# Optimization experiments

Hardware: AMD Instinct MI355X
Metric: run time of the kernel (lower is better)

Reference implementation:

```python
import jax, jax.numpy as jnp
import numpy as np

# ---- module hyperparams (match init_kwargs) ----
REGIONS_DIMS = [0, 1, 2, 4, 9, 16]
ALL_DIM = sum(REGIONS_DIMS)          # 32
NUM_REGIONS = len(REGIONS_DIMS)      # 6
FIELD_NUM = 32
VOCAB = 200000
BATCH = 8192
TEMPERATURE = 1.0
EPS = 1e-5                            # torch BatchNorm1d default eps


def _build_region_mask():
    """Replicates init_variables(): row 0 is all-zero (drop-feature region),
    rows 1..R-1 are disjoint consecutive segments of sizes REGIONS_DIMS[1:]."""
    mask = np.zeros((NUM_REGIONS, ALL_DIM), dtype=np.float32)
    dims_pre_sum = [0] + [sum(REGIONS_DIMS[1:i]) for i in range(2, NUM_REGIONS)]
    for r, (pre, dim) in enumerate(zip(dims_pre_sum, REGIONS_DIMS[1:]), start=1):
        mask[r, pre:pre + dim] = 1.0
    return jnp.asarray(mask)


def setup_inputs() -> dict:
    key = jax.random.key(0)
    k_ids, k_emb, k_w = jax.random.split(key, 3)
    input_ids = jax.random.randint(k_ids, (BATCH, FIELD_NUM), 0, VOCAB, dtype=jnp.int64)
    # torch.nn.init.uniform_(a=-0.05, b=0.05)
    emb_table = jax.random.uniform(k_emb, (VOCAB, ALL_DIM), dtype=jnp.float32,
                                   minval=-0.05, maxval=0.05)
    # xavier_uniform on [F, R, 1]: bound = sqrt(6/(R+1))
    bound = float(np.sqrt(6.0 / (NUM_REGIONS + 1)))
    field_region_weights = jax.random.uniform(
        k_w, (FIELD_NUM, NUM_REGIONS, 1), dtype=jnp.float32, minval=-bound, maxval=bound)
    return {
        "input_ids": input_ids,
        "emb_table": emb_table,
        "field_region_weights": field_region_weights,
        "region_mask": _build_region_mask(),
    }


def reference(input_ids, emb_table, field_region_weights, region_mask):
    # Embedding gather: [B, F, D]
    emb = emb_table[input_ids]
    # BatchNorm1d(field_num, affine=False), training mode: per-field stats over (batch, D),
    # biased variance (torch normalizes with biased var).
    mean = jnp.mean(emb, axis=(0, 2), keepdims=True)
    var = jnp.var(emb, axis=(0, 2), keepdims=True)
    x = (emb - mean) * jax.lax.rsqrt(var + EPS)
    # softmax over regions: [F, R]
    w = jax.nn.softmax(field_region_weights[..., 0] / TEMPERATURE, axis=1)
    # sum_r w[f,r] * mask[r,d] -> per-(field, dim) scale; equivalent to the original's
    # broadcast-to-[B,F,R,D], multiply, and sum over R, without the big intermediate.
    coef = jnp.einsum('fr,rd->fd', w, region_mask)
    return x * coef[None, :, :]
```

## Files before the change

kernel.cpp:

```cpp
#include <hip/hip_runtime.h>
#include <math.h>

#define BATCH    8192
#define FIELDS   32
#define DIM      32
#define NREG     6
#define EPS      1e-5f


__global__ void irazor_init_kernel(const float* __restrict__ frw,
                                   const float* __restrict__ mask,
                                   float* __restrict__ ws) {
    const int t = threadIdx.x;
    if (t < 64) ws[t] = 0.0f;
    __shared__ float smask[NREG * DIM];
    if (t < NREG * DIM) smask[t] = mask[t];
    __syncthreads();
    if (t < FIELDS) {
        float w[NREG];
        float m = -1e30f;
        #pragma unroll
        for (int r = 0; r < NREG; ++r) {
            w[r] = frw[t * NREG + r];
            m = fmaxf(m, w[r]);
        }
        float s = 0.0f;
        #pragma unroll
        for (int r = 0; r < NREG; ++r) { w[r] = __expf(w[r] - m); s += w[r]; }
        const float inv = 1.0f / s;
        for (int d = 0; d < DIM; ++d) {
            float c = 0.0f;
            #pragma unroll
            for (int r = 0; r < NREG; ++r) c += w[r] * smask[r * DIM + d];
            ws[64 + t * DIM + d] = c * inv;
        }
    }
}

__global__ __launch_bounds__(256) void irazor_stats_kernel(
        const int* __restrict__ ids,
        const float* __restrict__ table,
        float* __restrict__ ws) {
    const int f    = blockIdx.y;
    const int b0   = blockIdx.x * 256;
    const int t    = threadIdx.x;
    const int rsub = t >> 3;
    const int vec  = t & 7;

    float s = 0.0f, sq = 0.0f;
    #pragma unroll
    for (int i = 0; i < 8; ++i) {
        const int b  = b0 + i * 32 + rsub;
        const int id = ids[b * FIELDS + f];
        const float4 v = *reinterpret_cast<const float4*>(
            table + (size_t)id * DIM + vec * 4);
        s  += v.x + v.y + v.z + v.w;
        sq += v.x * v.x + v.y * v.y + v.z * v.z + v.w * v.w;
    }

    #pragma unroll
    for (int off = 1; off < 64; off <<= 1) {
        s  += __shfl_xor(s, off);
        sq += __shfl_xor(sq, off);
    }
    __shared__ float ls[4], lq[4];
    const int wave = t >> 6;
    if ((t & 63) == 0) { ls[wave] = s; lq[wave] = sq; }
    __syncthreads();
    if (t == 0) {
        const float S  = ls[0] + ls[1] + ls[2] + ls[3];
        const float SQ = lq[0] + lq[1] + lq[2] + lq[3];
        atomicAdd(&ws[f], S);
        atomicAdd(&ws[32 + f], SQ);
    }
}

__global__ __launch_bounds__(256) void irazor_out_kernel(
        const int* __restrict__ ids,
        const float* __restrict__ table,
        const float* __restrict__ ws,
        float* __restrict__ out) {
    const float* __restrict__ coef = ws + 64;
    const float invN = 1.0f / (float)(BATCH * DIM);
    const size_t total = (size_t)BATCH * FIELDS * (DIM / 4);
    for (size_t e = (size_t)blockIdx.x * blockDim.x + threadIdx.x; e < total;
         e += (size_t)gridDim.x * blockDim.x) {
        const int r   = (int)(e >> 3);
        const int vec = (int)(e & 7);
        const int f   = r & (FIELDS - 1);
        const int id  = ids[r];
        const float4 v = *reinterpret_cast<const float4*>(
            table + (size_t)id * DIM + vec * 4);
        const float S    = ws[f];
        const float SQ   = ws[32 + f];
        const float mean = S * invN;
        const float var  = SQ * invN - mean * mean;
        const float istd = rsqrtf(var + EPS);
        const float4 c = *reinterpret_cast<const float4*>(coef + f * DIM + vec * 4);
        float4 o;
        o.x = (v.x - mean) * istd * c.x;
        o.y = (v.y - mean) * istd * c.y;
        o.z = (v.z - mean) * istd * c.z;
        o.w = (v.w - mean) * istd * c.w;
        reinterpret_cast<float4*>(out)[e] = o;
    }
}

extern "C" void kernel_launch(void* const* d_in, const int* in_sizes, int n_in,
                              void* d_out, int out_size, void* d_ws, size_t ws_size,
                              hipStream_t stream) {
    const int*   ids   = (const int*)d_in[0];
    const float* table = (const float*)d_in[1];
    const float* frw   = (const float*)d_in[2];
    const float* mask  = (const float*)d_in[3];
    float*       out   = (float*)d_out;
    float*       ws    = (float*)d_ws;

    irazor_init_kernel<<<1, 256, 0, stream>>>(frw, mask, ws);

    dim3 sgrid(BATCH / 256, FIELDS);
    irazor_stats_kernel<<<sgrid, 256, 0, stream>>>(ids, table, ws);

    irazor_out_kernel<<<2048, 256, 0, stream>>>(ids, table, ws, out);
}
```

Before: 105.4 us.

## Fuse coefficient computation into output kernel and restructure stats reduction per field

Removes the separate init kernel by zeroing the accumulators with a memset and computing the softmax-masked coefficients inside each output block into shared memory. Both stats and output kernels now map each block to 8 batch rows across all fields, with one thread group of 8 per field. The stats kernel drops the block-wide reduction and issues atomics per field group instead. This saves a launch and simplifies indexing, but greatly increases the number of atomics onto 64 addresses and adds redundant coefficient work per block.

```diff
diff --git a/kernel.cpp b/kernel.cpp
--- a/kernel.cpp
+++ b/kernel.cpp
@@ -6,52 +6,22 @@
 #define DIM      32
 #define NREG     6
 #define EPS      1e-5f
+#define NBLK     1024
 
 
-__global__ void irazor_init_kernel(const float* __restrict__ frw,
-                                   const float* __restrict__ mask,
-                                   float* __restrict__ ws) {
-    const int t = threadIdx.x;
-    if (t < 64) ws[t] = 0.0f;
-    __shared__ float smask[NREG * DIM];
-    if (t < NREG * DIM) smask[t] = mask[t];
-    __syncthreads();
-    if (t < FIELDS) {
-        float w[NREG];
-        float m = -1e30f;
-        #pragma unroll
-        for (int r = 0; r < NREG; ++r) {
-            w[r] = frw[t * NREG + r];
-            m = fmaxf(m, w[r]);
-        }
-        float s = 0.0f;
-        #pragma unroll
-        for (int r = 0; r < NREG; ++r) { w[r] = __expf(w[r] - m); s += w[r]; }
-        const float inv = 1.0f / s;
-        for (int d = 0; d < DIM; ++d) {
-            float c = 0.0f;
-            #pragma unroll
-            for (int r = 0; r < NREG; ++r) c += w[r] * smask[r * DIM + d];
-            ws[64 + t * DIM + d] = c * inv;
-        }
-    }
-}
+__global__ __launch_bounds__(256) void irazor_stats_kernel(
+        const int*   __restrict__ ids,
+        const float* __restrict__ table,
+        float*       __restrict__ ws) {
+    const int t   = threadIdx.x;
+    const int blk = blockIdx.x;
+    const int f   = t >> 3;
+    const int vec = t & 7;
 
-__global__ __launch_bounds__(256) void irazor_stats_kernel(
-        const int* __restrict__ ids,
-        const float* __restrict__ table,
-        float* __restrict__ ws) {
-    const int f    = blockIdx.y;
-    const int b0   = blockIdx.x * 256;
-    const int t    = threadIdx.x;
-    const int rsub = t >> 3;
-    const int vec  = t & 7;
-
-    float s = 0.0f, sq = 0.0f;
+    float s = 0.f, sq = 0.f;
     #pragma unroll
     for (int i = 0; i < 8; ++i) {
-        const int b  = b0 + i * 32 + rsub;
-        const int id = ids[b * FIELDS + f];
+        const int id = ids[(blk * 8 + i) * FIELDS + f];
         const float4 v = *reinterpret_cast<const float4*>(
             table + (size_t)id * DIM + vec * 4);
         s  += v.x + v.y + v.z + v.w;
@@ -59,50 +29,68 @@
     }
 
     #pragma unroll
-    for (int off = 1; off < 64; off <<= 1) {
+    for (int off = 1; off < 8; off <<= 1) {
         s  += __shfl_xor(s, off);
         sq += __shfl_xor(sq, off);
     }
-    __shared__ float ls[4], lq[4];
-    const int wave = t >> 6;
-    if ((t & 63) == 0) { ls[wave] = s; lq[wave] = sq; }
-    __syncthreads();
-    if (t == 0) {
-        const float S  = ls[0] + ls[1] + ls[2] + ls[3];
-        const float SQ = lq[0] + lq[1] + lq[2] + lq[3];
-        atomicAdd(&ws[f], S);
-        atomicAdd(&ws[32 + f], SQ);
+    if (vec == 0) {
+        atomicAdd(&ws[f], s);
+        atomicAdd(&ws[32 + f], sq);
     }
 }
 
 __global__ __launch_bounds__(256) void irazor_out_kernel(
-        const int* __restrict__ ids,
+        const int*   __restrict__ ids,
         const float* __restrict__ table,
+        const float* __restrict__ frw,
+        const float* __restrict__ mask,
         const float* __restrict__ ws,
-        float* __restrict__ out) {
-    const float* __restrict__ coef = ws + 64;
-    const float invN = 1.0f / (float)(BATCH * DIM);
-    const size_t total = (size_t)BATCH * FIELDS * (DIM / 4);
-    for (size_t e = (size_t)blockIdx.x * blockDim.x + threadIdx.x; e < total;
-         e += (size_t)gridDim.x * blockDim.x) {
-        const int r   = (int)(e >> 3);
-        const int vec = (int)(e & 7);
-        const int f   = r & (FIELDS - 1);
-        const int id  = ids[r];
+        float*       __restrict__ out) {
+    const int t   = threadIdx.x;
+    const int blk = blockIdx.x;
+
+    __shared__ float scoef[FIELDS][DIM];
+    {
+        const int f2 = t & 31;
+        const int q  = t >> 5;
+        float w[NREG]; float m = -1e30f;
+        #pragma unroll
+        for (int r = 0; r < NREG; ++r) { w[r] = frw[f2 * NREG + r]; m = fmaxf(m, w[r]); }
+        float ssum = 0.f;
+        #pragma unroll
+        for (int r = 0; r < NREG; ++r) { w[r] = __expf(w[r] - m); ssum += w[r]; }
+        const float inv = 1.f / ssum;
+        #pragma unroll
+        for (int dd = 0; dd < 4; ++dd) {
+            const int d = q * 4 + dd;
+            float c = 0.f;
+            #pragma unroll
+            for (int r = 0; r < NREG; ++r) c += w[r] * mask[r * DIM + d];
+            scoef[f2][d] = c * inv;
+        }
+    }
+    __syncthreads();
+
+    const int f   = t >> 3;
+    const int vec = t & 7;
+    const float invN = 1.f / (float)(BATCH * DIM);
+    const float mean = ws[f] * invN;
+    const float var  = ws[32 + f] * invN - mean * mean;
+    const float istd = rsqrtf(var + EPS);
+    const float4 c = *reinterpret_cast<const float4*>(&scoef[f][vec * 4]);
+
+    float4* __restrict__ out4 = reinterpret_cast<float4*>(out);
+    #pragma unroll
+    for (int i = 0; i < 8; ++i) {
+        const int id = ids[(blk * 8 + i) * FIELDS + f];
         const float4 v = *reinterpret_cast<const float4*>(
             table + (size_t)id * DIM + vec * 4);
-        const float S    = ws[f];
-        const float SQ   = ws[32 + f];
-        const float mean = S * invN;
-        const float var  = SQ * invN - mean * mean;
-        const float istd = rsqrtf(var + EPS);
-        const float4 c = *reinterpret_cast<const float4*>(coef + f * DIM + vec * 4);
         float4 o;
         o.x = (v.x - mean) * istd * c.x;
         o.y = (v.y - mean) * istd * c.y;
         o.z = (v.z - mean) * istd * c.z;
         o.w = (v.w - mean) * istd * c.w;
-        reinterpret_cast<float4*>(out)[e] = o;
+        out4[(size_t)blk * 2048 + (size_t)i * 256 + t] = o;
     }
 }
 
@@ -116,10 +104,7 @@
     float*       out   = (float*)d_out;
     float*       ws    = (float*)d_ws;
 
-    irazor_init_kernel<<<1, 256, 0, stream>>>(frw, mask, ws);
-
-    dim3 sgrid(BATCH / 256, FIELDS);
-    irazor_stats_kernel<<<sgrid, 256, 0, stream>>>(ids, table, ws);
-
-    irazor_out_kernel<<<2048, 256, 0, stream>>>(ids, table, ws, out);
+    hipMemsetAsync(ws, 0, 64 * sizeof(float), stream);
+    irazor_stats_kernel<<<NBLK, 256, 0, stream>>>(ids, table, ws);
+    irazor_out_kernel<<<NBLK, 256, 0, stream>>>(ids, table, frw, mask, ws, out);
 }
```

Result: slower. 141.0 us (+33.8%).
